# Kernel tuning notes

Hardware: AMD Instinct MI355X
Metric: run time of the kernel (lower is better)

Reference implementation:

```python
import jax, jax.numpy as jnp
import numpy as np
from jax import lax

B, T, V, E, H = 1024, 16, 8000, 256, 512


def setup_inputs() -> dict:
    key = jax.random.key(0)
    ks = jax.random.split(key, 9)
    return {
        "context": jax.random.normal(ks[0], (B, H), jnp.float32),
        "target_encs": jax.random.randint(ks[1], (B, T), 0, V, dtype=jnp.int32),
        "embed": jax.random.normal(ks[2], (V, E), jnp.float32) * 0.02,
        "W_ih": jax.random.normal(ks[3], (3 * H, E), jnp.float32) * 0.05,
        "W_hh": jax.random.normal(ks[4], (3 * H, H), jnp.float32) * 0.05,
        "b_ih": jnp.zeros((3 * H,), jnp.float32),
        "b_hh": jnp.zeros((3 * H,), jnp.float32),
        "out_W": jax.random.normal(ks[5], (V, H), jnp.float32) * 0.05,
        "out_b": jnp.zeros((V,), jnp.float32),
    }


def reference(context, target_encs, embed, W_ih, W_hh, b_ih, b_hh, out_W, out_b):
    # Teacher-forcing decode: initial hidden = context, first input token = token 0 (SOS).
    def gru_step(h, x):
        # x: (B, E), h: (B, H). PyTorch GRU gate math, gates ordered [r, z, n].
        gi = x @ W_ih.T + b_ih          # (B, 3H)
        gh = h @ W_hh.T + b_hh          # (B, 3H)
        i_r, i_z, i_n = jnp.split(gi, 3, axis=-1)
        h_r, h_z, h_n = jnp.split(gh, 3, axis=-1)
        r = jax.nn.sigmoid(i_r + h_r)
        z = jax.nn.sigmoid(i_z + h_z)
        n = jnp.tanh(i_n + r * h_n)
        h_new = (1.0 - z) * n + z * h
        logp = jax.nn.log_softmax(h_new @ out_W.T + out_b, axis=-1)  # (B, V)
        return h_new, logp

    bos = jnp.broadcast_to(embed[0], (1, B, E))              # SOS embedding for every sample
    tgt_emb = jnp.swapaxes(embed[target_encs], 0, 1)         # (T, B, E)
    xs = jnp.concatenate([bos, tgt_emb[: T - 1]], axis=0)    # inputs shifted right by one
    _, logps = lax.scan(gru_step, context, xs)                # (T, B, V)
    return jnp.swapaxes(logps, 0, 1)                          # (B, T, V)
```

## Files before the change

### kernel.cpp

```cpp
#include <hip/hip_runtime.h>
#include <hip/hip_bf16.h>

using bf16 = __hip_bfloat16;
typedef __attribute__((ext_vector_type(8))) short short8v;
typedef __attribute__((ext_vector_type(4))) float float4v;

#define B_SZ 1024
#define T_SZ 16
#define V_SZ 8000
#define E_SZ 256
#define H_SZ 512
#define KSTEP 768
#define NSTEP 2048
#define NROWS (B_SZ * T_SZ)
#define NTILES_V 63

typedef const __attribute__((address_space(1))) void* gas_ptr;
typedef __attribute__((address_space(3))) void* las_ptr;

__device__ __forceinline__ void async16(void* lds, const void* g) {
  __builtin_amdgcn_global_load_lds((gas_ptr)g, (las_ptr)lds, 16, 0, 0);
}

__global__ __launch_bounds__(256) void prep_kernel(
    const float* __restrict__ ctx, const float* __restrict__ embed,
    const float* __restrict__ W_ih, const float* __restrict__ W_hh,
    const float* __restrict__ b_ih, const float* __restrict__ b_hh,
    const float* __restrict__ outW,
    bf16* __restrict__ Wbig, float* __restrict__ biasB,
    bf16* __restrict__ embB, bf16* __restrict__ outWB,
    bf16* __restrict__ ctxB, float* __restrict__ hF)
{
  const int total = 2048*768 + 2048 + 8000*256 + 8000*512 + 1024*512 + 1024*512;
  int i = blockIdx.x * 256 + threadIdx.x;
  if (i >= total) return;
  int idx = i;
  if (idx < 2048*768) {
    int n = idx / 768, k = idx % 768;
    int h = n >> 2, g = n & 3;
    float v;
    if (g < 3) v = (k < E_SZ) ? W_ih[(g*H_SZ + h)*E_SZ + k]
                              : W_hh[(g*H_SZ + h)*H_SZ + (k - E_SZ)];
    else       v = (k < E_SZ) ? 0.f
                              : W_hh[(2*H_SZ + h)*H_SZ + (k - E_SZ)];
    Wbig[idx] = __float2bfloat16(v);
    return;
  }
  idx -= 2048*768;
  if (idx < 2048) {
    int h = idx >> 2, g = idx & 3;
    biasB[idx] = (g < 3) ? (b_ih[g*H_SZ + h] + b_hh[g*H_SZ + h]) : b_hh[2*H_SZ + h];
    return;
  }
  idx -= 2048;
  if (idx < 8000*256) { embB[idx] = __float2bfloat16(embed[idx]); return; }
  idx -= 8000*256;
  if (idx < 8000*512) { outWB[idx] = __float2bfloat16(outW[idx]); return; }
  idx -= 8000*512;
  if (idx < 1024*512) { ctxB[idx] = __float2bfloat16(ctx[idx]); return; }
  idx -= 1024*512;
  hF[idx] = ctx[idx];
}

__global__ __launch_bounds__(256) void step_kernel(
    const bf16* __restrict__ Wbig, const float* __restrict__ biasB,
    const bf16* __restrict__ embB, const int* __restrict__ tok,
    const bf16* __restrict__ ctxB, bf16* __restrict__ hist,
    float* __restrict__ hF, int t)
{
  __shared__ bf16 As[128*32];
  __shared__ bf16 Bs[128*32];
  __shared__ bf16 Cs[128*132];

  const int tid = threadIdx.x;
  const int lane = tid & 63, wave = tid >> 6;
  const int m0 = blockIdx.x * 128;
  const int n0 = blockIdx.y * 128;
  const int mw = (wave & 1) * 64, nw = (wave >> 1) * 64;

  float4v acc[4][4];
#pragma unroll
  for (int i = 0; i < 4; i++)
#pragma unroll
    for (int j = 0; j < 4; j++) acc[i][j] = (float4v){0.f, 0.f, 0.f, 0.f};

  const bf16* hsrc = (t == 0) ? ctxB : (hist + (size_t)(t - 1) * H_SZ);
  const size_t hstride = (t == 0) ? (size_t)H_SZ : (size_t)T_SZ * H_SZ;

  for (int kc = 0; kc < KSTEP; kc += 32) {
#pragma unroll
    for (int p = 0; p < 2; p++) {
      int flat = (p * 256 + tid) * 8;
      int r = flat >> 5, c = flat & 31;
      const bf16* srcA;
      if (kc < E_SZ) {
        int tk = (t == 0) ? 0 : tok[(m0 + r) * T_SZ + (t - 1)];
        srcA = embB + (size_t)tk * E_SZ + kc + c;
      } else {
        srcA = hsrc + (size_t)(m0 + r) * hstride + (kc - E_SZ) + c;
      }
      async16(&As[flat], srcA);
      async16(&Bs[flat], Wbig + (size_t)(n0 + r) * KSTEP + kc + c);
    }
    __syncthreads();
    short8v a[4], b[4];
#pragma unroll
    for (int i = 0; i < 4; i++)
      a[i] = *(const short8v*)&As[(mw + i * 16 + (lane & 15)) * 32 + (lane >> 4) * 8];
#pragma unroll
    for (int j = 0; j < 4; j++)
      b[j] = *(const short8v*)&Bs[(nw + j * 16 + (lane & 15)) * 32 + (lane >> 4) * 8];
#pragma unroll
    for (int i = 0; i < 4; i++)
#pragma unroll
      for (int j = 0; j < 4; j++)
        acc[i][j] = __builtin_amdgcn_mfma_f32_16x16x32_bf16(a[i], b[j], acc[i][j], 0, 0, 0);
    __syncthreads();
  }

#pragma unroll
  for (int i = 0; i < 4; i++)
#pragma unroll
    for (int j = 0; j < 4; j++)
#pragma unroll
      for (int r = 0; r < 4; r++) {
        int row = mw + i * 16 + ((lane >> 4) << 2) + r;
        int col = nw + j * 16 + (lane & 15);
        Cs[row * 132 + col] = __float2bfloat16(acc[i][j][r]);
      }
  __syncthreads();

  for (int p = 0; p < 16; p++) {
    int idx = p * 256 + tid;
    int h = idx & 31, brow = idx >> 5;
    int bg = m0 + brow;
    int hg = (n0 >> 2) + h;
    const bf16* cp = &Cs[brow * 132 + h * 4];
    const float* bp = &biasB[n0 + h * 4];
    float c0 = __bfloat162float(cp[0]) + bp[0];
    float c1 = __bfloat162float(cp[1]) + bp[1];
    float c2 = __bfloat162float(cp[2]) + bp[2];
    float c3 = __bfloat162float(cp[3]) + bp[3];
    float r = 1.f / (1.f + __expf(-c0));
    float z = 1.f / (1.f + __expf(-c1));
    float n = tanhf(c2 + (r - 1.f) * c3);
    float hp = hF[(size_t)bg * H_SZ + hg];
    float hnew = (1.f - z) * n + z * hp;
    hF[(size_t)bg * H_SZ + hg] = hnew;
    hist[((size_t)bg * T_SZ + t) * H_SZ + hg] = __float2bfloat16(hnew);
  }
}

__global__ __launch_bounds__(256) void logits_kernel(
    const bf16* __restrict__ hist, const bf16* __restrict__ outWB,
    const float* __restrict__ outb, float* __restrict__ out,
    float* __restrict__ pmax, float* __restrict__ psum)
{
  __shared__ bf16 As[128*32];
  __shared__ bf16 Bs[128*32];
  __shared__ float redM[128][2];
  __shared__ float redS[128][2];

  const int tid = threadIdx.x;
  const int lane = tid & 63, wave = tid >> 6;
  const int nt = blockIdx.x;
  const int m0 = blockIdx.y * 128;
  const int n0 = nt * 128;
  const int mw = (wave & 1) * 64, nw = (wave >> 1) * 64;

  float4v acc[4][4];
#pragma unroll
  for (int i = 0; i < 4; i++)
#pragma unroll
    for (int j = 0; j < 4; j++) acc[i][j] = (float4v){0.f, 0.f, 0.f, 0.f};

  for (int kc = 0; kc < H_SZ; kc += 32) {
#pragma unroll
    for (int p = 0; p < 2; p++) {
      int flat = (p * 256 + tid) * 8;
      int r = flat >> 5, c = flat & 31;
      async16(&As[flat], hist + (size_t)(m0 + r) * H_SZ + kc + c);
      int nr = n0 + r; if (nr > V_SZ - 1) nr = V_SZ - 1;
      async16(&Bs[flat], outWB + (size_t)nr * H_SZ + kc + c);
    }
    __syncthreads();
    short8v a[4], b[4];
#pragma unroll
    for (int i = 0; i < 4; i++)
      a[i] = *(const short8v*)&As[(mw + i * 16 + (lane & 15)) * 32 + (lane >> 4) * 8];
#pragma unroll
    for (int j = 0; j < 4; j++)
      b[j] = *(const short8v*)&Bs[(nw + j * 16 + (lane & 15)) * 32 + (lane >> 4) * 8];
#pragma unroll
    for (int i = 0; i < 4; i++)
#pragma unroll
      for (int j = 0; j < 4; j++)
        acc[i][j] = __builtin_amdgcn_mfma_f32_16x16x32_bf16(a[i], b[j], acc[i][j], 0, 0, 0);
    __syncthreads();
  }

  const float NEG = -1e30f;
  float ob[4]; bool valid[4];
#pragma unroll
  for (int j = 0; j < 4; j++) {
    int n = n0 + nw + j * 16 + (lane & 15);
    valid[j] = (n < V_SZ);
    ob[j] = valid[j] ? outb[n] : 0.f;
  }

  float m_[4][4], s_[4][4];
#pragma unroll
  for (int i = 0; i < 4; i++)
#pragma unroll
    for (int r = 0; r < 4; r++) { m_[i][r] = NEG; s_[i][r] = 0.f; }

#pragma unroll
  for (int i = 0; i < 4; i++) {
    int row = m0 + mw + i * 16 + ((lane >> 4) << 2);
#pragma unroll
    for (int j = 0; j < 4; j++) {
      int n = n0 + nw + j * 16 + (lane & 15);
#pragma unroll
      for (int r = 0; r < 4; r++) {
        float v = acc[i][j][r] + ob[j];
        acc[i][j][r] = v;
        if (valid[j]) {
          out[(size_t)(row + r) * V_SZ + n] = v;
          m_[i][r] = fmaxf(m_[i][r], v);
        }
      }
    }
  }
#pragma unroll
  for (int i = 0; i < 4; i++)
#pragma unroll
    for (int r = 0; r < 4; r++) {
#pragma unroll
      for (int d = 1; d < 16; d <<= 1)
        m_[i][r] = fmaxf(m_[i][r], __shfl_xor(m_[i][r], d));
    }
#pragma unroll
  for (int i = 0; i < 4; i++)
#pragma unroll
    for (int j = 0; j < 4; j++)
#pragma unroll
      for (int r = 0; r < 4; r++)
        if (valid[j]) s_[i][r] += __expf(acc[i][j][r] - m_[i][r]);
#pragma unroll
  for (int i = 0; i < 4; i++)
#pragma unroll
    for (int r = 0; r < 4; r++) {
#pragma unroll
      for (int d = 1; d < 16; d <<= 1)
        s_[i][r] += __shfl_xor(s_[i][r], d);
    }
  if ((lane & 15) == 0) {
#pragma unroll
    for (int i = 0; i < 4; i++)
#pragma unroll
      for (int r = 0; r < 4; r++) {
        int rl = mw + i * 16 + ((lane >> 4) << 2) + r;
        redM[rl][nw >> 6] = m_[i][r];
        redS[rl][nw >> 6] = s_[i][r];
      }
  }
  __syncthreads();
  if (tid < 128) {
    float M0v = redM[tid][0], M1v = redM[tid][1];
    float S0v = redS[tid][0], S1v = redS[tid][1];
    float M = fmaxf(M0v, M1v);
    float S = S0v * __expf(M0v - M) + S1v * __expf(M1v - M);
    pmax[(size_t)nt * NROWS + m0 + tid] = M;
    psum[(size_t)nt * NROWS + m0 + tid] = S;
  }
}

__global__ __launch_bounds__(256) void lse_kernel(
    const float* __restrict__ pmax, const float* __restrict__ psum,
    float* __restrict__ lse)
{
  int r = blockIdx.x * 256 + threadIdx.x;
  if (r >= NROWS) return;
  float M = -1e30f, S = 0.f;
  for (int c = 0; c < NTILES_V; c++) {
    float m = pmax[(size_t)c * NROWS + r];
    float s = psum[(size_t)c * NROWS + r];
    if (m > M) { S = S * __expf(M - m) + s; M = m; }
    else       { S += s * __expf(m - M); }
  }
  lse[r] = M + logf(S);
}

__global__ __launch_bounds__(256) void sub_kernel(
    float* __restrict__ out, const float* __restrict__ lse)
{
  const int total4 = B_SZ * T_SZ * V_SZ / 4;
  int i = blockIdx.x * 256 + threadIdx.x;
  if (i >= total4) return;
  float4 v = ((float4*)out)[i];
  int row = (i * 4) / V_SZ;
  float l = lse[row];
  v.x -= l; v.y -= l; v.z -= l; v.w -= l;
  ((float4*)out)[i] = v;
}

extern "C" void kernel_launch(void* const* d_in, const int* in_sizes, int n_in,
                              void* d_out, int out_size, void* d_ws, size_t ws_size,
                              hipStream_t stream)
{
  const float* ctx   = (const float*)d_in[0];
  const int*   tok   = (const int*)d_in[1];
  const float* embed = (const float*)d_in[2];
  const float* W_ih  = (const float*)d_in[3];
  const float* W_hh  = (const float*)d_in[4];
  const float* b_ih  = (const float*)d_in[5];
  const float* b_hh  = (const float*)d_in[6];
  const float* outW  = (const float*)d_in[7];
  const float* outb  = (const float*)d_in[8];
  float* out = (float*)d_out;

  char* base = (char*)d_ws;
  size_t o = 0;
  auto take = [&](size_t nbytes) -> void* {
    void* r = base + o;
    o = (o + nbytes + 255) & ~(size_t)255;
    return r;
  };
  bf16*  Wbig  = (bf16*) take((size_t)NSTEP * KSTEP * 2);
  float* biasB = (float*)take((size_t)NSTEP * 4);
  bf16*  embB  = (bf16*) take((size_t)V_SZ * E_SZ * 2);
  bf16*  outWB = (bf16*) take((size_t)V_SZ * H_SZ * 2);
  bf16*  ctxB  = (bf16*) take((size_t)B_SZ * H_SZ * 2);
  float* hF    = (float*)take((size_t)B_SZ * H_SZ * 4);
  bf16*  hist  = (bf16*) take((size_t)NROWS * H_SZ * 2);
  float* pmax  = (float*)take((size_t)NTILES_V * NROWS * 4);
  float* psum  = (float*)take((size_t)NTILES_V * NROWS * 4);
  float* lse   = (float*)take((size_t)NROWS * 4);

  {
    int total = 2048*768 + 2048 + 8000*256 + 8000*512 + 1024*512 + 1024*512;
    prep_kernel<<<(total + 255) / 256, 256, 0, stream>>>(
        ctx, embed, W_ih, W_hh, b_ih, b_hh, outW,
        Wbig, biasB, embB, outWB, ctxB, hF);
  }
  for (int t = 0; t < T_SZ; t++) {
    step_kernel<<<dim3(8, 16), 256, 0, stream>>>(
        Wbig, biasB, embB, tok, ctxB, hist, hF, t);
  }
  logits_kernel<<<dim3(NTILES_V, NROWS / 128), 256, 0, stream>>>(
      hist, outWB, outb, out, pmax, psum);
  lse_kernel<<<(NROWS + 255) / 256, 256, 0, stream>>>(pmax, psum, lse);
  {
    int total4 = B_SZ * T_SZ * V_SZ / 4;
    sub_kernel<<<(total4 + 255) / 256, 256, 0, stream>>>(out, lse);
  }
}
```

Measured before the change: 1.316 ms.

## Hoist input-gate GEMM out of recurrence, shrink step tiles, store bf16 logits

The input-to-hidden projection for all timesteps is precomputed in one large GEMM (gi_kernel) over pre-gathered embeddings. Each recurrent step then only runs the 512-deep hidden GEMM, using 64-row tiles so more blocks are launched, and keeps gate sums in fp32 LDS. Logits are written as padded bf16 to a scratch buffer, and the final subtract pass reads bf16 and writes fp32 output, which cuts logits-write traffic. In exchange there is a 128MB fp32 Gi buffer to write and read, and logits lose precision before the log-softmax subtraction.

```diff
diff --git a/kernel.cpp b/kernel.cpp
--- a/kernel.cpp
+++ b/kernel.cpp
@@ -10,10 +10,11 @@
 #define V_SZ 8000
 #define E_SZ 256
 #define H_SZ 512
-#define KSTEP 768
+#define KW 768
 #define NSTEP 2048
 #define NROWS (B_SZ * T_SZ)
 #define NTILES_V 63
+#define LPAD 8064
 
 typedef const __attribute__((address_space(1))) void* gas_ptr;
 typedef __attribute__((address_space(3))) void* las_ptr;
@@ -22,21 +23,30 @@
   __builtin_amdgcn_global_load_lds((gas_ptr)g, (las_ptr)lds, 16, 0, 0);
 }
 
+__device__ __forceinline__ float bfu2f(unsigned short u) {
+  unsigned int x = ((unsigned int)u) << 16;
+  return __uint_as_float(x);
+}
+
 __global__ __launch_bounds__(256) void prep_kernel(
-    const float* __restrict__ ctx, const float* __restrict__ embed,
+    const float* __restrict__ ctx, const int* __restrict__ tok,
+    const float* __restrict__ embed,
     const float* __restrict__ W_ih, const float* __restrict__ W_hh,
     const float* __restrict__ b_ih, const float* __restrict__ b_hh,
     const float* __restrict__ outW,
     bf16* __restrict__ Wbig, float* __restrict__ biasB,
-    bf16* __restrict__ embB, bf16* __restrict__ outWB,
+    bf16* __restrict__ X, bf16* __restrict__ outWB,
     bf16* __restrict__ ctxB, float* __restrict__ hF)
 {
-  const int total = 2048*768 + 2048 + 8000*256 + 8000*512 + 1024*512 + 1024*512;
-  int i = blockIdx.x * 256 + threadIdx.x;
-  if (i >= total) return;
-  int idx = i;
-  if (idx < 2048*768) {
-    int n = idx / 768, k = idx % 768;
+  const int N1 = NSTEP * KW;
+  const int N2 = NSTEP;
+  const int N3 = NROWS * E_SZ;
+  const int N4 = V_SZ * H_SZ;
+  const int N5 = B_SZ * H_SZ;
+  const int N6 = B_SZ * H_SZ;
+  int idx = blockIdx.x * 256 + threadIdx.x;
+  if (idx < N1) {
+    int n = idx / KW, k = idx % KW;
     int h = n >> 2, g = n & 3;
     float v;
     if (g < 3) v = (k < E_SZ) ? W_ih[(g*H_SZ + h)*E_SZ + k]
@@ -46,32 +56,35 @@
     Wbig[idx] = __float2bfloat16(v);
     return;
   }
-  idx -= 2048*768;
-  if (idx < 2048) {
+  idx -= N1;
+  if (idx < N2) {
     int h = idx >> 2, g = idx & 3;
     biasB[idx] = (g < 3) ? (b_ih[g*H_SZ + h] + b_hh[g*H_SZ + h]) : b_hh[2*H_SZ + h];
     return;
   }
-  idx -= 2048;
-  if (idx < 8000*256) { embB[idx] = __float2bfloat16(embed[idx]); return; }
-  idx -= 8000*256;
-  if (idx < 8000*512) { outWB[idx] = __float2bfloat16(outW[idx]); return; }
-  idx -= 8000*512;
-  if (idx < 1024*512) { ctxB[idx] = __float2bfloat16(ctx[idx]); return; }
-  idx -= 1024*512;
-  hF[idx] = ctx[idx];
-}
-
-__global__ __launch_bounds__(256) void step_kernel(
-    const bf16* __restrict__ Wbig, const float* __restrict__ biasB,
-    const bf16* __restrict__ embB, const int* __restrict__ tok,
-    const bf16* __restrict__ ctxB, bf16* __restrict__ hist,
-    float* __restrict__ hF, int t)
+  idx -= N2;
+  if (idx < N3) {
+    int e = idx & (E_SZ - 1);
+    int rb = idx >> 8;
+    int t = rb >> 10, b = rb & (B_SZ - 1);
+    int tk = (t == 0) ? 0 : tok[b * T_SZ + (t - 1)];
+    X[idx] = __float2bfloat16(embed[(size_t)tk * E_SZ + e]);
+    return;
+  }
+  idx -= N3;
+  if (idx < N4) { outWB[idx] = __float2bfloat16(outW[idx]); return; }
+  idx -= N4;
+  if (idx < N5) { ctxB[idx] = __float2bfloat16(ctx[idx]); return; }
+  idx -= N5;
+  if (idx < N6) hF[idx] = ctx[idx];
+}
+
+__global__ __launch_bounds__(256) void gi_kernel(
+    const bf16* __restrict__ X, const bf16* __restrict__ Wbig,
+    const float* __restrict__ biasB, float* __restrict__ Gi)
 {
   __shared__ bf16 As[128*32];
   __shared__ bf16 Bs[128*32];
-  __shared__ bf16 Cs[128*132];
-
   const int tid = threadIdx.x;
   const int lane = tid & 63, wave = tid >> 6;
   const int m0 = blockIdx.x * 128;
@@ -84,23 +97,13 @@
 #pragma unroll
     for (int j = 0; j < 4; j++) acc[i][j] = (float4v){0.f, 0.f, 0.f, 0.f};
 
-  const bf16* hsrc = (t == 0) ? ctxB : (hist + (size_t)(t - 1) * H_SZ);
-  const size_t hstride = (t == 0) ? (size_t)H_SZ : (size_t)T_SZ * H_SZ;
-
-  for (int kc = 0; kc < KSTEP; kc += 32) {
+  for (int kc = 0; kc < E_SZ; kc += 32) {
 #pragma unroll
     for (int p = 0; p < 2; p++) {
       int flat = (p * 256 + tid) * 8;
       int r = flat >> 5, c = flat & 31;
-      const bf16* srcA;
-      if (kc < E_SZ) {
-        int tk = (t == 0) ? 0 : tok[(m0 + r) * T_SZ + (t - 1)];
-        srcA = embB + (size_t)tk * E_SZ + kc + c;
-      } else {
-        srcA = hsrc + (size_t)(m0 + r) * hstride + (kc - E_SZ) + c;
-      }
-      async16(&As[flat], srcA);
-      async16(&Bs[flat], Wbig + (size_t)(n0 + r) * KSTEP + kc + c);
+      async16(&As[flat], X + (size_t)(m0 + r) * E_SZ + kc + c);
+      async16(&Bs[flat], Wbig + (size_t)(n0 + r) * KW + kc + c);
     }
     __syncthreads();
     short8v a[4], b[4];
@@ -117,33 +120,101 @@
         acc[i][j] = __builtin_amdgcn_mfma_f32_16x16x32_bf16(a[i], b[j], acc[i][j], 0, 0, 0);
     __syncthreads();
   }
-
-#pragma unroll
-  for (int i = 0; i < 4; i++)
-#pragma unroll
-    for (int j = 0; j < 4; j++)
+#pragma unroll
+  for (int j = 0; j < 4; j++) {
+    int n = n0 + nw + j * 16 + (lane & 15);
+    float bias = biasB[n];
+#pragma unroll
+    for (int i = 0; i < 4; i++) {
+      int row = m0 + mw + i * 16 + ((lane >> 4) << 2);
+#pragma unroll
+      for (int r = 0; r < 4; r++)
+        Gi[(size_t)(row + r) * NSTEP + n] = acc[i][j][r] + bias;
+    }
+  }
+}
+
+__global__ __launch_bounds__(256) void step_kernel(
+    const bf16* __restrict__ Wbig, const float* __restrict__ Gi,
+    const bf16* __restrict__ ctxB, bf16* __restrict__ hist,
+    float* __restrict__ hF, int t)
+{
+  __shared__ bf16 As[64*32];
+  __shared__ bf16 Bs[128*32];
+  __shared__ float Cs[64*132];
+
+  const int tid = threadIdx.x;
+  const int lane = tid & 63, wave = tid >> 6;
+  const int m0 = blockIdx.x * 64;
+  const int n0 = blockIdx.y * 128;
+
+  float4v acc[4][2];
+#pragma unroll
+  for (int i = 0; i < 4; i++)
+#pragma unroll
+    for (int j = 0; j < 2; j++) acc[i][j] = (float4v){0.f, 0.f, 0.f, 0.f};
+
+  const bf16* hsrc = (t == 0) ? (ctxB + (size_t)m0 * H_SZ)
+                              : (hist + ((size_t)m0 * T_SZ + (t - 1)) * H_SZ);
+  const size_t hstride = (t == 0) ? (size_t)H_SZ : (size_t)T_SZ * H_SZ;
+
+  for (int kc = 0; kc < H_SZ; kc += 32) {
+    {
+      int flat = tid * 8;
+      int r = flat >> 5, c = flat & 31;
+      async16(&As[flat], hsrc + (size_t)r * hstride + kc + c);
+    }
+#pragma unroll
+    for (int p = 0; p < 2; p++) {
+      int flat = (p * 256 + tid) * 8;
+      int r = flat >> 5, c = flat & 31;
+      async16(&Bs[flat], Wbig + (size_t)(n0 + r) * KW + E_SZ + kc + c);
+    }
+    __syncthreads();
+    short8v a[4], b[2];
+#pragma unroll
+    for (int i = 0; i < 4; i++)
+      a[i] = *(const short8v*)&As[(i * 16 + (lane & 15)) * 32 + (lane >> 4) * 8];
+#pragma unroll
+    for (int j = 0; j < 2; j++)
+      b[j] = *(const short8v*)&Bs[(wave * 32 + j * 16 + (lane & 15)) * 32 + (lane >> 4) * 8];
+#pragma unroll
+    for (int i = 0; i < 4; i++)
+#pragma unroll
+      for (int j = 0; j < 2; j++)
+        acc[i][j] = __builtin_amdgcn_mfma_f32_16x16x32_bf16(a[i], b[j], acc[i][j], 0, 0, 0);
+    __syncthreads();
+  }
+
+#pragma unroll
+  for (int i = 0; i < 4; i++)
+#pragma unroll
+    for (int j = 0; j < 2; j++)
 #pragma unroll
       for (int r = 0; r < 4; r++) {
-        int row = mw + i * 16 + ((lane >> 4) << 2) + r;
-        int col = nw + j * 16 + (lane & 15);
-        Cs[row * 132 + col] = __float2bfloat16(acc[i][j][r]);
+        int row = i * 16 + ((lane >> 4) << 2) + r;
+        int col = wave * 32 + j * 16 + (lane & 15);
+        Cs[row * 132 + col] = acc[i][j][r];
       }
   __syncthreads();
 
-  for (int p = 0; p < 16; p++) {
+#pragma unroll
+  for (int p = 0; p < 8; p++) {
     int idx = p * 256 + tid;
     int h = idx & 31, brow = idx >> 5;
     int bg = m0 + brow;
     int hg = (n0 >> 2) + h;
-    const bf16* cp = &Cs[brow * 132 + h * 4];
-    const float* bp = &biasB[n0 + h * 4];
-    float c0 = __bfloat162float(cp[0]) + bp[0];
-    float c1 = __bfloat162float(cp[1]) + bp[1];
-    float c2 = __bfloat162float(cp[2]) + bp[2];
-    float c3 = __bfloat162float(cp[3]) + bp[3];
-    float r = 1.f / (1.f + __expf(-c0));
-    float z = 1.f / (1.f + __expf(-c1));
-    float n = tanhf(c2 + (r - 1.f) * c3);
+    const float4* gi4 = (const float4*)&Gi[((size_t)t * B_SZ + bg) * NSTEP + n0 + h * 4];
+    float4 g = *gi4;
+    const float4* ch4 = (const float4*)&Cs[brow * 132 + h * 4];
+    float4 ch = *ch4;
+    float c0 = g.x + ch.x;
+    float c1 = g.y + ch.y;
+    float c2 = g.z + ch.z;
+    float c3 = g.w + ch.w;
+    float r_ = 1.f / (1.f + __expf(-c0));
+    float z  = 1.f / (1.f + __expf(-c1));
+    float n  = tanhf(c2 + (r_ - 1.f) * c3);
     float hp = hF[(size_t)bg * H_SZ + hg];
     float hnew = (1.f - z) * n + z * hp;
     hF[(size_t)bg * H_SZ + hg] = hnew;
@@ -153,7 +224,7 @@
 
 __global__ __launch_bounds__(256) void logits_kernel(
     const bf16* __restrict__ hist, const bf16* __restrict__ outWB,
-    const float* __restrict__ outb, float* __restrict__ out,
+    const float* __restrict__ outb, bf16* __restrict__ L,
     float* __restrict__ pmax, float* __restrict__ psum)
 {
   __shared__ bf16 As[128*32];
@@ -224,10 +295,8 @@
       for (int r = 0; r < 4; r++) {
         float v = acc[i][j][r] + ob[j];
         acc[i][j][r] = v;
-        if (valid[j]) {
-          out[(size_t)(row + r) * V_SZ + n] = v;
-          m_[i][r] = fmaxf(m_[i][r], v);
-        }
+        L[(size_t)(row + r) * LPAD + n] = __float2bfloat16(v);
+        if (valid[j]) m_[i][r] = fmaxf(m_[i][r], v);
       }
     }
   }
@@ -292,16 +361,28 @@
 }
 
 __global__ __launch_bounds__(256) void sub_kernel(
-    float* __restrict__ out, const float* __restrict__ lse)
-{
-  const int total4 = B_SZ * T_SZ * V_SZ / 4;
+    const unsigned short* __restrict__ L, const float* __restrict__ lse,
+    float* __restrict__ out)
+{
+  const int total8 = NROWS * (V_SZ / 8);
   int i = blockIdx.x * 256 + threadIdx.x;
-  if (i >= total4) return;
-  float4 v = ((float4*)out)[i];
-  int row = (i * 4) / V_SZ;
+  if (i >= total8) return;
+  int row = i / (V_SZ / 8);
+  int c = (i - row * (V_SZ / 8)) * 8;
   float l = lse[row];
-  v.x -= l; v.y -= l; v.z -= l; v.w -= l;
-  ((float4*)out)[i] = v;
+  short8v v = *(const short8v*)&L[(size_t)row * LPAD + c];
+  float4 o0, o1;
+  o0.x = bfu2f((unsigned short)v[0]) - l;
+  o0.y = bfu2f((unsigned short)v[1]) - l;
+  o0.z = bfu2f((unsigned short)v[2]) - l;
+  o0.w = bfu2f((unsigned short)v[3]) - l;
+  o1.x = bfu2f((unsigned short)v[4]) - l;
+  o1.y = bfu2f((unsigned short)v[5]) - l;
+  o1.z = bfu2f((unsigned short)v[6]) - l;
+  o1.w = bfu2f((unsigned short)v[7]) - l;
+  float4* op = (float4*)&out[(size_t)row * V_SZ + c];
+  op[0] = o0;
+  op[1] = o1;
 }
 
 extern "C" void kernel_launch(void* const* d_in, const int* in_sizes, int n_in,
@@ -326,32 +407,36 @@
     o = (o + nbytes + 255) & ~(size_t)255;
     return r;
   };
-  bf16*  Wbig  = (bf16*) take((size_t)NSTEP * KSTEP * 2);
+  bf16*  Wbig  = (bf16*) take((size_t)NSTEP * KW * 2);
   float* biasB = (float*)take((size_t)NSTEP * 4);
-  bf16*  embB  = (bf16*) take((size_t)V_SZ * E_SZ * 2);
+  bf16*  X     = (bf16*) take((size_t)NROWS * E_SZ * 2);
   bf16*  outWB = (bf16*) take((size_t)V_SZ * H_SZ * 2);
   bf16*  ctxB  = (bf16*) take((size_t)B_SZ * H_SZ * 2);
   float* hF    = (float*)take((size_t)B_SZ * H_SZ * 4);
   bf16*  hist  = (bf16*) take((size_t)NROWS * H_SZ * 2);
+  float* Gi    = (float*)take((size_t)NROWS * NSTEP * 4);
+  bf16*  L     = (bf16*) take((size_t)NROWS * LPAD * 2);
   float* pmax  = (float*)take((size_t)NTILES_V * NROWS * 4);
   float* psum  = (float*)take((size_t)NTILES_V * NROWS * 4);
   float* lse   = (float*)take((size_t)NROWS * 4);
 
   {
-    int total = 2048*768 + 2048 + 8000*256 + 8000*512 + 1024*512 + 1024*512;
+    int total = NSTEP*KW + NSTEP + NROWS*E_SZ + V_SZ*H_SZ + B_SZ*H_SZ + B_SZ*H_SZ;
     prep_kernel<<<(total + 255) / 256, 256, 0, stream>>>(
-        ctx, embed, W_ih, W_hh, b_ih, b_hh, outW,
-        Wbig, biasB, embB, outWB, ctxB, hF);
-  }
+        ctx, tok, embed, W_ih, W_hh, b_ih, b_hh, outW,
+        Wbig, biasB, X, outWB, ctxB, hF);
+  }
+  gi_kernel<<<dim3(NROWS / 128, NSTEP / 128), 256, 0, stream>>>(X, Wbig, biasB, Gi);
   for (int t = 0; t < T_SZ; t++) {
-    step_kernel<<<dim3(8, 16), 256, 0, stream>>>(
-        Wbig, biasB, embB, tok, ctxB, hist, hF, t);
+    step_kernel<<<dim3(B_SZ / 64, NSTEP / 128), 256, 0, stream>>>(
+        Wbig, Gi, ctxB, hist, hF, t);
   }
   logits_kernel<<<dim3(NTILES_V, NROWS / 128), 256, 0, stream>>>(
-      hist, outWB, outb, out, pmax, psum);
+      hist, outWB, outb, L, pmax, psum);
   lse_kernel<<<(NROWS + 255) / 256, 256, 0, stream>>>(pmax, psum, lse);
   {
-    int total4 = B_SZ * T_SZ * V_SZ / 4;
-    sub_kernel<<<(total4 + 255) / 256, 256, 0, stream>>>(out, lse);
-  }
-}
+    int total8 = NROWS * (V_SZ / 8);
+    sub_kernel<<<(total8 + 255) / 256, 256, 0, stream>>>(
+        (const unsigned short*)L, lse, out);
+  }
+}
```

New measurement: 1.115 ms. 15.3% less time.
